# Optimization experiments

Hardware: AMD Instinct MI355X
Metric: run time of the kernel (lower is better)

Reference implementation:

```python
import jax, jax.numpy as jnp
import numpy as np

GROUP_SIZE = 128


def _unpack_int4(packed):
    # packed: [..., P] int32, each holding 8 int4 nibbles (LSB-first).
    u = jax.lax.bitcast_convert_type(packed, jnp.uint32)
    shifts = jnp.arange(8, dtype=jnp.uint32) * 4  # nibble bit offsets
    vals = (u[..., None] >> shifts) & jnp.uint32(15)  # [..., P, 8]
    return vals.reshape(*packed.shape[:-1], -1)  # [..., P*8] in [0, 15]


def setup_inputs() -> dict:
    key = jax.random.key(0)
    k1, k2, k3, k4 = jax.random.split(key, 4)
    B, S, K, O = 4, 16, 4096, 11008
    G = K // GROUP_SIZE          # 32 groups
    GP = (G + 7) // 8            # 4 packed-zero columns
    imax = np.iinfo(np.int32).max
    x = jax.random.normal(k1, (B, S, K), dtype=jnp.float16)
    qweight_i32 = jax.random.randint(k2, (O, K // 8), 0, imax, dtype=jnp.int32)
    qzeros_i32 = jax.random.randint(k3, (O, GP), 0, imax, dtype=jnp.int32)
    scales_f16 = jax.random.uniform(k4, (O, G), dtype=jnp.float16,
                                    minval=0.001, maxval=0.02)
    return {"x": x, "qweight_i32": qweight_i32, "qzeros_i32": qzeros_i32,
            "scales_f16": scales_f16}


def reference(x, qweight_i32, qzeros_i32, scales_f16):
    O, G = scales_f16.shape
    K = G * GROUP_SIZE
    # Dequantize: w = (q - z) * s, per-group int4 quantization.
    q = _unpack_int4(qweight_i32)[:, :K].astype(jnp.float16)       # [O, K]
    z = _unpack_int4(qzeros_i32)[:, :G].astype(jnp.float16)        # [O, G]
    z_k = jnp.repeat(z, GROUP_SIZE, axis=1)                        # [O, K]
    s_k = jnp.repeat(scales_f16, GROUP_SIZE, axis=1)               # [O, K]
    w = (q - z_k) * s_k                                            # fp16 [O, K]
    x2d = x.reshape(-1, K).astype(jnp.float16)                     # [m, K]
    out = jnp.matmul(x2d, w.T).astype(jnp.float32)                 # [m, O]
    return out.reshape(*x.shape[:-1], O)
```

## Files before the change

kernel.cpp:

```cpp
#include <hip/hip_runtime.h>
#include <stdint.h>

typedef _Float16 half8  __attribute__((ext_vector_type(8)));
typedef float    floatx4 __attribute__((ext_vector_type(4)));
typedef uint32_t uint4v  __attribute__((ext_vector_type(4)));

#define KDIM 4096
#define ODIM 11008
#define NG   32

__device__ __forceinline__ uint32_t pk_f16(float a, float b) {
    return __builtin_bit_cast(uint32_t, __builtin_amdgcn_cvt_pkrtz(a, b));
}

__global__ __launch_bounds__(256) void cvt_x_kernel(
    const float4* __restrict__ x, uint4v* __restrict__ xh2,
    float* __restrict__ xsumT)
{
    const int i = blockIdx.x * 256 + threadIdx.x;
    const float4 f0 = x[2 * i];
    const float4 f1 = x[2 * i + 1];
    const uint4v v = {pk_f16(f0.x, f1.x), pk_f16(f0.y, f1.y),
                      pk_f16(f0.z, f1.z), pk_f16(f0.w, f1.w)};
    const int m  = i >> 9, c = i & 511;
    const int g  = c >> 4, cg = c & 15, q = cg >> 2, ks = cg & 3;
    const int mt = m >> 4, ml = m & 15;
    xh2[((size_t)(g * 4 + ks) * 4 + mt) * 64 + q * 16 + ml] = v;

    float p = f0.x + f0.y + f0.z + f0.w + f1.x + f1.y + f1.z + f1.w;
    p += __shfl_xor(p, 1);
    p += __shfl_xor(p, 2);
    p += __shfl_xor(p, 4);
    p += __shfl_xor(p, 8);
    if ((threadIdx.x & 15) == 0) xsumT[g * 64 + m] = p;
}

__global__ __launch_bounds__(256, 2) void w4a16_kernel(
    const uint4v*   __restrict__ xh2,
    const uint4v*   __restrict__ qw,
    const uint32_t* __restrict__ qz,
    const float*    __restrict__ sc,
    const float*    __restrict__ xsumT,
    float*          __restrict__ out)
{
    __shared__ float red[4][16][64];

    const int t    = threadIdx.x;
    const int kw   = t >> 6;
    const int lane = t & 63;
    const int q    = lane >> 4;
    const int ml   = lane & 15;

    const int o0 = blockIdx.x * 16;
    const int o  = o0 + ml;
    const int g0 = kw * 8;

    const uint4v* qwp = qw + (size_t)o * 128 + g0 * 4 + q;
    const uint32_t zdw = qz[(size_t)o * 4 + kw];
    const floatx4 sv0 = *reinterpret_cast<const floatx4*>(sc + (size_t)o * NG + g0);
    const floatx4 sv1 = *reinterpret_cast<const floatx4*>(sc + (size_t)o * NG + g0 + 4);

    const uint4v* xp = xh2 + (size_t)g0 * 1024 + lane;
    const float*  xs = xsumT + (size_t)g0 * 64 + q * 4;

    floatx4 acc[4] = {{0.f,0.f,0.f,0.f},{0.f,0.f,0.f,0.f},
                      {0.f,0.f,0.f,0.f},{0.f,0.f,0.f,0.f}};

    uint4v ubuf[2];
    ubuf[0] = qwp[0];
    ubuf[1] = qwp[4];

    #pragma unroll 1
    for (int gl = 0; gl < 8; ++gl) {
        const uint4v ucur = ubuf[gl & 1];
        if (gl + 2 < 8) ubuf[gl & 1] = qwp[(gl + 2) * 4];

        const uint32_t zn  = (zdw >> (gl * 4)) & 0xFu;
        const float    s   = (gl < 4) ? sv0[gl] : sv1[gl - 4];
        const float    czs = s * (1024.0f + (float)zn);

        floatx4 tmp[4] = {{0.f,0.f,0.f,0.f},{0.f,0.f,0.f,0.f},
                          {0.f,0.f,0.f,0.f},{0.f,0.f,0.f,0.f}};

        #pragma unroll
        for (int h = 0; h < 2; ++h) {
            uint4v ax[8];
            #pragma unroll
            for (int i = 0; i < 8; ++i)
                ax[i] = xp[(size_t)(gl * 16 + h * 8 + i) * 64];

            #pragma unroll
            for (int k2 = 0; k2 < 2; ++k2) {
                const int ks = h * 2 + k2;
                const uint32_t ud = ucur[ks];
                const uint4v bw = {
                    ( ud         & 0x000F000Fu) | 0x64006400u,
                    ((ud >> 4)   & 0x000F000Fu) | 0x64006400u,
                    ((ud >> 8)   & 0x000F000Fu) | 0x64006400u,
                    ((ud >> 12)  & 0x000F000Fu) | 0x64006400u};
                const half8 b = __builtin_bit_cast(half8, bw);
                #pragma unroll
                for (int mt = 0; mt < 4; ++mt)
                    tmp[mt] = __builtin_amdgcn_mfma_f32_16x16x32_f16(
                        __builtin_bit_cast(half8, ax[k2 * 4 + mt]), b, tmp[mt],
                        0, 0, 0);
            }
        }

        #pragma unroll
        for (int mt = 0; mt < 4; ++mt) {
            const floatx4 xg = *reinterpret_cast<const floatx4*>(
                xs + gl * 64 + mt * 16);
            #pragma unroll
            for (int r = 0; r < 4; ++r)
                acc[mt][r] += s * tmp[mt][r] - czs * xg[r];
        }
    }

    #pragma unroll
    for (int mt = 0; mt < 4; ++mt)
        #pragma unroll
        for (int r = 0; r < 4; ++r)
            red[kw][mt * 4 + r][lane] = acc[mt][r];
    __syncthreads();

    const int mt2 = t >> 6;
    #pragma unroll
    for (int r = 0; r < 4; ++r) {
        const int i = mt2 * 4 + r;
        const float sum = red[0][i][lane] + red[1][i][lane]
                        + red[2][i][lane] + red[3][i][lane];
        out[(size_t)(mt2 * 16 + q * 4 + r) * ODIM + o] = sum;
    }
}

extern "C" void kernel_launch(void* const* d_in, const int* in_sizes, int n_in,
                              void* d_out, int out_size, void* d_ws, size_t ws_size,
                              hipStream_t stream) {
    const float*    x       = (const float*)d_in[0];
    const uint32_t* qweight = (const uint32_t*)d_in[1];
    const uint32_t* qzeros  = (const uint32_t*)d_in[2];
    const float*    scales  = (const float*)d_in[3];
    float* out = (float*)d_out;

    uint4v* xh2   = (uint4v*)d_ws;
    float*  xsumT = (float*)((char*)d_ws + 512 * 1024);

    cvt_x_kernel<<<dim3(128), dim3(256), 0, stream>>>((const float4*)x, xh2, xsumT);
    w4a16_kernel<<<dim3(ODIM / 16), dim3(256), 0, stream>>>(
        xh2, (const uint4v*)qweight, qzeros, scales, xsumT, out);
}
```

Measured before the change: 93.71 us.

## Switch to 32x32x16 MFMA tiles with split-K across blocks and atomic reduction

Moves the int4 GEMM from 16x16x32 to 32x32x16 MFMA instructions, with 32 output columns per block, and re-lays out the converted activations to match. K is split in two across block pairs, so the grid stays at 688 blocks with fewer groups per wave. Partial results are combined with atomicAdd into an output that an extra kernel zeroes first. This cuts per-MFMA B-operand dequant reuse overhead, but it adds a zeroing launch, atomic traffic and a non-deterministic summation order.

```diff
diff --git a/kernel.cpp b/kernel.cpp
--- a/kernel.cpp
+++ b/kernel.cpp
@@ -1,20 +1,34 @@
 #include <hip/hip_runtime.h>
 #include <stdint.h>
 
-typedef _Float16 half8  __attribute__((ext_vector_type(8)));
+typedef _Float16 half8   __attribute__((ext_vector_type(8)));
 typedef float    floatx4 __attribute__((ext_vector_type(4)));
+typedef float    floatx16 __attribute__((ext_vector_type(16)));
 typedef uint32_t uint4v  __attribute__((ext_vector_type(4)));
 
 #define KDIM 4096
 #define ODIM 11008
 #define NG   32
 
+__global__ void zero_out_kernel(float4* __restrict__ out) {
+    out[(size_t)blockIdx.x * 256 + threadIdx.x] = float4{0.f, 0.f, 0.f, 0.f};
+}
+
 __device__ __forceinline__ uint32_t pk_f16(float a, float b) {
     return __builtin_bit_cast(uint32_t, __builtin_amdgcn_cvt_pkrtz(a, b));
 }
 
+__device__ __forceinline__ half8 dq(uint32_t ud) {
+    const uint4v bw = {
+        ( ud         & 0x000F000Fu) | 0x64006400u,
+        ((ud >> 4)   & 0x000F000Fu) | 0x64006400u,
+        ((ud >> 8)   & 0x000F000Fu) | 0x64006400u,
+        ((ud >> 12)  & 0x000F000Fu) | 0x64006400u};
+    return __builtin_bit_cast(half8, bw);
+}
+
 __global__ __launch_bounds__(256) void cvt_x_kernel(
-    const float4* __restrict__ x, uint4v* __restrict__ xh2,
+    const float4* __restrict__ x, uint4v* __restrict__ xh3,
     float* __restrict__ xsumT)
 {
     const int i = blockIdx.x * 256 + threadIdx.x;
@@ -23,9 +37,9 @@
     const uint4v v = {pk_f16(f0.x, f1.x), pk_f16(f0.y, f1.y),
                       pk_f16(f0.z, f1.z), pk_f16(f0.w, f1.w)};
     const int m  = i >> 9, c = i & 511;
-    const int g  = c >> 4, cg = c & 15, q = cg >> 2, ks = cg & 3;
-    const int mt = m >> 4, ml = m & 15;
-    xh2[((size_t)(g * 4 + ks) * 4 + mt) * 64 + q * 16 + ml] = v;
+    const int g  = c >> 4, cg = c & 15, h = cg >> 3, ks = cg & 7;
+    const int mt = m >> 5, ml = m & 31;
+    xh3[((size_t)(g * 8 + ks) * 2 + mt) * 64 + h * 32 + ml] = v;
 
     float p = f0.x + f0.y + f0.z + f0.w + f1.x + f1.y + f1.z + f1.w;
     p += __shfl_xor(p, 1);
@@ -36,101 +50,93 @@
 }
 
 __global__ __launch_bounds__(256, 2) void w4a16_kernel(
-    const uint4v*   __restrict__ xh2,
+    const uint4v*   __restrict__ xh3,
     const uint4v*   __restrict__ qw,
     const uint32_t* __restrict__ qz,
     const float*    __restrict__ sc,
     const float*    __restrict__ xsumT,
     float*          __restrict__ out)
 {
-    __shared__ float red[4][16][64];
+    __shared__ float red[4][2048];
 
     const int t    = threadIdx.x;
     const int kw   = t >> 6;
     const int lane = t & 63;
-    const int q    = lane >> 4;
-    const int ml   = lane & 15;
+    const int h    = lane >> 5;
+    const int ml   = lane & 31;
 
-    const int o0 = blockIdx.x * 16;
+    const int kb = blockIdx.x & 1;
+    const int ob = blockIdx.x >> 1;
+    const int o0 = ob * 32;
     const int o  = o0 + ml;
-    const int g0 = kw * 8;
+    const int g0 = kb * 16 + kw * 4;
 
-    const uint4v* qwp = qw + (size_t)o * 128 + g0 * 4 + q;
-    const uint32_t zdw = qz[(size_t)o * 4 + kw];
-    const floatx4 sv0 = *reinterpret_cast<const floatx4*>(sc + (size_t)o * NG + g0);
-    const floatx4 sv1 = *reinterpret_cast<const floatx4*>(sc + (size_t)o * NG + g0 + 4);
+    const uint4v* qwp = qw + (size_t)o * 128 + g0 * 4 + h * 2;
+    const uint32_t zdw = qz[(size_t)o * 4 + (g0 >> 3)];
+    const int zsh = (g0 & 7) * 4;
+    const floatx4 sv = *reinterpret_cast<const floatx4*>(sc + (size_t)o * NG + g0);
 
-    const uint4v* xp = xh2 + (size_t)g0 * 1024 + lane;
-    const float*  xs = xsumT + (size_t)g0 * 64 + q * 4;
+    const uint4v* xp = xh3 + (size_t)g0 * 16 * 64 + lane;
 
-    floatx4 acc[4] = {{0.f,0.f,0.f,0.f},{0.f,0.f,0.f,0.f},
-                      {0.f,0.f,0.f,0.f},{0.f,0.f,0.f,0.f}};
+    floatx16 acc[2] = {};
 
-    uint4v ubuf[2];
-    ubuf[0] = qwp[0];
-    ubuf[1] = qwp[4];
+    uint4v u0 = qwp[0], u1 = qwp[1];
 
     #pragma unroll 1
-    for (int gl = 0; gl < 8; ++gl) {
-        const uint4v ucur = ubuf[gl & 1];
-        if (gl + 2 < 8) ubuf[gl & 1] = qwp[(gl + 2) * 4];
+    for (int gi = 0; gi < 4; ++gi) {
+        const uint4v c0 = u0, c1 = u1;
+        if (gi + 1 < 4) { u0 = qwp[(gi + 1) * 4]; u1 = qwp[(gi + 1) * 4 + 1]; }
 
-        const uint32_t zn  = (zdw >> (gl * 4)) & 0xFu;
-        const float    s   = (gl < 4) ? sv0[gl] : sv1[gl - 4];
-        const float    czs = s * (1024.0f + (float)zn);
+        const int   g   = g0 + gi;
+        const float s   = sv[gi];
+        const uint32_t zn = (zdw >> (zsh + gi * 4)) & 0xFu;
+        const float czs = s * (1024.0f + (float)zn);
 
-        floatx4 tmp[4] = {{0.f,0.f,0.f,0.f},{0.f,0.f,0.f,0.f},
-                          {0.f,0.f,0.f,0.f},{0.f,0.f,0.f,0.f}};
+        half8 b[8];
+        #pragma unroll
+        for (int ks = 0; ks < 4; ++ks) { b[ks] = dq(c0[ks]); b[4 + ks] = dq(c1[ks]); }
 
         #pragma unroll
-        for (int h = 0; h < 2; ++h) {
+        for (int mt = 0; mt < 2; ++mt) {
             uint4v ax[8];
             #pragma unroll
-            for (int i = 0; i < 8; ++i)
-                ax[i] = xp[(size_t)(gl * 16 + h * 8 + i) * 64];
+            for (int ks = 0; ks < 8; ++ks)
+                ax[ks] = xp[(size_t)(gi * 16 + ks * 2 + mt) * 64];
+
+            floatx16 tmp = {};
+            #pragma unroll
+            for (int ks = 0; ks < 8; ++ks)
+                tmp = __builtin_amdgcn_mfma_f32_32x32x16_f16(
+                    __builtin_bit_cast(half8, ax[ks]), b[ks], tmp, 0, 0, 0);
 
             #pragma unroll
-            for (int k2 = 0; k2 < 2; ++k2) {
-                const int ks = h * 2 + k2;
-                const uint32_t ud = ucur[ks];
-                const uint4v bw = {
-                    ( ud         & 0x000F000Fu) | 0x64006400u,
-                    ((ud >> 4)   & 0x000F000Fu) | 0x64006400u,
-                    ((ud >> 8)   & 0x000F000Fu) | 0x64006400u,
-                    ((ud >> 12)  & 0x000F000Fu) | 0x64006400u};
-                const half8 b = __builtin_bit_cast(half8, bw);
+            for (int rr = 0; rr < 4; ++rr) {
+                const floatx4 xsg = *reinterpret_cast<const floatx4*>(
+                    xsumT + g * 64 + mt * 32 + rr * 8 + h * 4);
                 #pragma unroll
-                for (int mt = 0; mt < 4; ++mt)
-                    tmp[mt] = __builtin_amdgcn_mfma_f32_16x16x32_f16(
-                        __builtin_bit_cast(half8, ax[k2 * 4 + mt]), b, tmp[mt],
-                        0, 0, 0);
+                for (int j = 0; j < 4; ++j)
+                    acc[mt][rr * 4 + j] += s * tmp[rr * 4 + j] - czs * xsg[j];
             }
-        }
-
-        #pragma unroll
-        for (int mt = 0; mt < 4; ++mt) {
-            const floatx4 xg = *reinterpret_cast<const floatx4*>(
-                xs + gl * 64 + mt * 16);
-            #pragma unroll
-            for (int r = 0; r < 4; ++r)
-                acc[mt][r] += s * tmp[mt][r] - czs * xg[r];
         }
     }
 
     #pragma unroll
-    for (int mt = 0; mt < 4; ++mt)
+    for (int mt = 0; mt < 2; ++mt)
         #pragma unroll
-        for (int r = 0; r < 4; ++r)
-            red[kw][mt * 4 + r][lane] = acc[mt][r];
+        for (int rr = 0; rr < 4; ++rr)
+            #pragma unroll
+            for (int j = 0; j < 4; ++j) {
+                const int m = mt * 32 + rr * 8 + h * 4 + j;
+                red[kw][m * 32 + ml] = acc[mt][rr * 4 + j];
+            }
     __syncthreads();
 
-    const int mt2 = t >> 6;
     #pragma unroll
-    for (int r = 0; r < 4; ++r) {
-        const int i = mt2 * 4 + r;
-        const float sum = red[0][i][lane] + red[1][i][lane]
-                        + red[2][i][lane] + red[3][i][lane];
-        out[(size_t)(mt2 * 16 + q * 4 + r) * ODIM + o] = sum;
+    for (int r = 0; r < 8; ++r) {
+        const int i  = r * 256 + t;
+        const int m  = i >> 5, ol = i & 31;
+        const float v = red[0][i] + red[1][i] + red[2][i] + red[3][i];
+        atomicAdd(out + (size_t)m * ODIM + o0 + ol, v);
     }
 }
 
@@ -143,10 +149,11 @@
     const float*    scales  = (const float*)d_in[3];
     float* out = (float*)d_out;
 
-    uint4v* xh2   = (uint4v*)d_ws;
+    uint4v* xh3   = (uint4v*)d_ws;
     float*  xsumT = (float*)((char*)d_ws + 512 * 1024);
 
-    cvt_x_kernel<<<dim3(128), dim3(256), 0, stream>>>((const float4*)x, xh2, xsumT);
-    w4a16_kernel<<<dim3(ODIM / 16), dim3(256), 0, stream>>>(
-        xh2, (const uint4v*)qweight, qzeros, scales, xsumT, out);
+    cvt_x_kernel<<<dim3(128), dim3(256), 0, stream>>>((const float4*)x, xh3, xsumT);
+    zero_out_kernel<<<dim3(688), dim3(256), 0, stream>>>((float4*)out);
+    w4a16_kernel<<<dim3(688), dim3(256), 0, stream>>>(
+        xh3, (const uint4v*)qweight, qzeros, scales, xsumT, out);
 }
```

After: 93.98 us. No clear change (+0.3%).
